# Kernel optimization log

Measured on AMD Instinct MI355X. Metric: run time of the kernel, lower is better.

## Reference

```python
import jax, jax.numpy as jnp
import numpy as np
from jax import lax

N = 100000      # nodes
E = 1600000     # edges
F_IN = 128      # nfeat
F_OUT = 32      # nhid


def _l2norm(v, eps=1e-12):
    return v / jnp.maximum(jnp.linalg.norm(v), eps)


def setup_inputs() -> dict:
    key = jax.random.key(0)
    k1, k2, k3, k4, k5 = jax.random.split(key, 5)
    x = jax.random.normal(k1, (N, F_IN), dtype=jnp.float32)
    edge_index = jax.random.randint(k2, (2, E), 0, N, dtype=jnp.int64)
    W = jax.random.normal(k3, (F_OUT, F_IN), dtype=jnp.float32) * (1.0 / np.sqrt(F_IN))
    bias = jax.random.normal(k4, (F_OUT,), dtype=jnp.float32) * 0.01
    prelu_a = jnp.full((1,), 0.25, dtype=jnp.float32)  # PReLU default init
    u_sn = jax.random.normal(k5, (F_OUT,), dtype=jnp.float32)
    return {"x": x, "edge_index": edge_index, "W": W, "bias": bias,
            "prelu_a": prelu_a, "u_sn": u_sn}


def _spectral_norm_weight(W, u):
    # one power iteration (torch default), u/v treated as buffers (no grad)
    v = lax.stop_gradient(_l2norm(W.T @ u))
    u2 = lax.stop_gradient(_l2norm(W @ v))
    sigma = jnp.dot(u2, W @ v)
    return W / sigma


def reference(x, edge_index, W, bias, prelu_a, u_sn):
    W_sn = _spectral_norm_weight(W, u_sn)
    # linear transform first (PyG GCNConv): [N, F_OUT]
    xw = x @ W_sn.T
    # add self loops
    loop = jnp.arange(N, dtype=edge_index.dtype)
    row = jnp.concatenate([edge_index[0], loop])  # source
    col = jnp.concatenate([edge_index[1], loop])  # target
    # symmetric normalization deg^{-1/2} A deg^{-1/2}, deg over targets
    deg = jax.ops.segment_sum(jnp.ones_like(col, dtype=xw.dtype), col, num_segments=N)
    dis = jnp.where(deg > 0, lax.rsqrt(deg), 0.0)
    norm = dis[row] * dis[col]                    # [E+N]
    # gather-scale-scatter aggregation
    msgs = xw[row] * norm[:, None]                # [E+N, F_OUT]
    out = jax.ops.segment_sum(msgs, col, num_segments=N)
    out = out + bias
    # PReLU with single shared slope
    a = prelu_a[0]
    return jnp.where(out >= 0, out, a * out)
```

## Files before the change

kernel.cpp:

```cpp
#include <hip/hip_runtime.h>
#include <hip/hip_fp16.h>

#define F_IN 128
#define F_OUT 32
#define PBLK 256
#define BSH 8

__global__ void k0_specnorm(const float* __restrict__ W, const float* __restrict__ u,
                            float* __restrict__ Wsc) {
    __shared__ float v[F_IN];
    __shared__ float red[F_IN];
    __shared__ float scal;
    int t = threadIdx.x;
    float acc = 0.f;
    for (int i = 0; i < F_OUT; ++i) acc += W[i * F_IN + t] * u[i];
    v[t] = acc;
    red[t] = acc * acc;
    __syncthreads();
    if (t == 0) {
        float s = 0.f;
        for (int i = 0; i < F_IN; ++i) s += red[i];
        scal = 1.0f / fmaxf(sqrtf(s), 1e-12f);
    }
    __syncthreads();
    v[t] = v[t] * scal;
    __syncthreads();
    if (t < F_OUT) {
        float a2 = 0.f;
        for (int j = 0; j < F_IN; ++j) a2 += W[t * F_IN + j] * v[j];
        red[t] = a2 * a2;
    }
    __syncthreads();
    if (t == 0) {
        float s = 0.f;
        for (int i = 0; i < F_OUT; ++i) s += red[i];
        scal = 1.0f / fmaxf(sqrtf(s), 1e-30f);
    }
    __syncthreads();
    float is = scal;
    for (int i = 0; i < F_OUT; ++i)
        Wsc[i * F_IN + t] = W[i * F_IN + t] * is;
}

__global__ __launch_bounds__(256) void k1_xw(const float* __restrict__ x,
                                             const float* __restrict__ Wsc,
                                             const float* __restrict__ dis,
                                             __half* __restrict__ xwh, int Nn) {
    __shared__ float xs[128 * 65];
    __shared__ float wt[128 * 32];
    int t = threadIdx.x;
    int rbase = blockIdx.x * 128;

    {
        int f = t >> 3;
        int kb = 16 * (t & 7);
        const float4* wrow = (const float4*)(Wsc + (size_t)f * F_IN + kb);
#pragma unroll
        for (int j = 0; j < 4; ++j) {
            float4 w = wrow[j];
            int k = kb + 4 * j;
            wt[(k + 0) * 32 + f] = w.x;
            wt[(k + 1) * 32 + f] = w.y;
            wt[(k + 2) * 32 + f] = w.z;
            wt[(k + 3) * 32 + f] = w.w;
        }
    }

    int r0 = (t >> 3) * 4;
    int f0 = (t & 7) * 4;
    float4 acc0 = {0, 0, 0, 0}, acc1 = {0, 0, 0, 0};
    float4 acc2 = {0, 0, 0, 0}, acc3 = {0, 0, 0, 0};
    const float4* wt4 = (const float4*)wt;
    int fq = f0 >> 2;

    for (int kc = 0; kc < 2; ++kc) {
        __syncthreads();
        {
            int rr = t >> 4;
            int k0 = 4 * (t & 15);
#pragma unroll
            for (int p = 0; p < 8; ++p) {
                int r = p * 16 + rr;
                int grow = rbase + r;
                if (grow >= Nn) grow = Nn - 1;
                float4 v = *(const float4*)(x + (size_t)grow * F_IN + kc * 64 + k0);
                xs[r * 65 + k0 + 0] = v.x;
                xs[r * 65 + k0 + 1] = v.y;
                xs[r * 65 + k0 + 2] = v.z;
                xs[r * 65 + k0 + 3] = v.w;
            }
        }
        __syncthreads();
#pragma unroll 4
        for (int kk = 0; kk < 64; ++kk) {
            int k = kc * 64 + kk;
            float4 w = wt4[k * 8 + fq];
            float x0 = xs[(r0 + 0) * 65 + kk];
            float x1 = xs[(r0 + 1) * 65 + kk];
            float x2 = xs[(r0 + 2) * 65 + kk];
            float x3 = xs[(r0 + 3) * 65 + kk];
            acc0.x += x0 * w.x; acc0.y += x0 * w.y; acc0.z += x0 * w.z; acc0.w += x0 * w.w;
            acc1.x += x1 * w.x; acc1.y += x1 * w.y; acc1.z += x1 * w.z; acc1.w += x1 * w.w;
            acc2.x += x2 * w.x; acc2.y += x2 * w.y; acc2.z += x2 * w.z; acc2.w += x2 * w.w;
            acc3.x += x3 * w.x; acc3.y += x3 * w.y; acc3.z += x3 * w.z; acc3.w += x3 * w.w;
        }
    }
    int g0 = rbase + r0;
#pragma unroll
    for (int q = 0; q < 4; ++q) {
        int g = g0 + q;
        if (g < Nn) {
            float d = dis[g];
            float4 a = (q == 0) ? acc0 : (q == 1) ? acc1 : (q == 2) ? acc2 : acc3;
            ushort4 s;
            s.x = __half_as_ushort(__float2half(a.x * d));
            s.y = __half_as_ushort(__float2half(a.y * d));
            s.z = __half_as_ushort(__float2half(a.z * d));
            s.w = __half_as_ushort(__float2half(a.w * d));
            *(ushort4*)(xwh + (size_t)g * F_OUT + f0) = s;
        }
    }
}

__global__ void k_hist(const int* __restrict__ col, int* __restrict__ M,
                       int E_, int NB) {
    __shared__ int h[512];
    int p = blockIdx.x, t = threadIdx.x;
    for (int b = t; b < NB; b += 256) h[b] = 0;
    __syncthreads();
    int epb = (E_ + PBLK - 1) / PBLK;
    int e0 = p * epb, e1 = min(e0 + epb, E_);
    for (int e = e0 + t; e < e1; e += 256)
        atomicAdd(&h[col[e] >> BSH], 1);
    __syncthreads();
    for (int b = t; b < NB; b += 256) M[b * PBLK + p] = h[b];
}

__global__ void k_scanA(int* __restrict__ M, int* __restrict__ total, int NB) {
    __shared__ int sd[256];
    int b = blockIdx.x, t = threadIdx.x;
    int v = M[b * PBLK + t];
    sd[t] = v;
    __syncthreads();
    for (int o = 1; o < 256; o <<= 1) {
        int u = (t >= o) ? sd[t - o] : 0;
        __syncthreads();
        sd[t] += u;
        __syncthreads();
    }
    M[b * PBLK + t] = sd[t] - v;
    if (t == 255) total[b] = sd[255];
}

__global__ void k_scanB(const int* __restrict__ total, int* __restrict__ base, int NB) {
    __shared__ int sd[512];
    int t = threadIdx.x;
    int v = (t < NB) ? total[t] : 0;
    sd[t] = v;
    __syncthreads();
    for (int o = 1; o < 512; o <<= 1) {
        int u = (t >= o) ? sd[t - o] : 0;
        __syncthreads();
        sd[t] += u;
        __syncthreads();
    }
    if (t < NB) base[t] = sd[t] - v;
    if (t == NB - 1) base[NB] = sd[t];
}

__global__ void k_scat1(const int* __restrict__ ei, const int* __restrict__ M,
                        const int* __restrict__ base, unsigned* __restrict__ staging,
                        int E_, int NB) {
    __shared__ int cur[512];
    int p = blockIdx.x, t = threadIdx.x;
    for (int b = t; b < NB; b += 256) cur[b] = base[b] + M[b * PBLK + p];
    __syncthreads();
    int epb = (E_ + PBLK - 1) / PBLK;
    int e0 = p * epb, e1 = min(e0 + epb, E_);
    for (int e = e0 + t; e < e1; e += 256) {
        int c = ei[E_ + e];
        int r = ei[e];
        int b = c >> BSH;
        int pos = atomicAdd(&cur[b], 1);
        staging[pos] = ((unsigned)r << BSH) | (unsigned)(c & 255);
    }
}

__global__ void k_sort2(const unsigned* __restrict__ staging, const int* __restrict__ base,
                        int* __restrict__ esr, float* __restrict__ dis,
                        int* __restrict__ cursor, int Nn, int E_, int NB) {
    __shared__ int hist[256];
    __shared__ int sd[256];
    __shared__ int lcur[256];
    int b = blockIdx.x, t = threadIdx.x;
    int nb0 = b << BSH;
    int nc = min(256, Nn - nb0);
    hist[t] = 0;
    __syncthreads();
    int s0 = base[b], s1 = base[b + 1];
    for (int j = s0 + t; j < s1; j += 256)
        atomicAdd(&hist[staging[j] & 255], 1);
    __syncthreads();
    int h = hist[t];
    if (t < nc) dis[nb0 + t] = rsqrtf((float)h + 1.0f);
    sd[t] = h;
    __syncthreads();
    for (int o = 1; o < 256; o <<= 1) {
        int u = (t >= o) ? sd[t - o] : 0;
        __syncthreads();
        sd[t] += u;
        __syncthreads();
    }
    int excl = sd[t] - h;
    if (t < nc) cursor[nb0 + t] = s0 + excl;
    if (b == NB - 1 && t == 0) cursor[Nn] = E_;
    lcur[t] = s0 + excl;
    __syncthreads();
    for (int j = s0 + t; j < s1; j += 256) {
        unsigned v = staging[j];
        int p = atomicAdd(&lcur[v & 255], 1);
        esr[p] = (int)(v >> BSH);
    }
}

__global__ void k4_gather(const int* __restrict__ esr, const int* __restrict__ cursor,
                          const __half* __restrict__ xws, const float* __restrict__ dis,
                          const float* __restrict__ bias, const float* __restrict__ pa,
                          float* __restrict__ out, int Nn) {
    int t = threadIdx.x;
    int node = blockIdx.x * 16 + (t >> 4);
    if (node >= Nn) return;
    int f2 = t & 15;
    int start = cursor[node], end = cursor[node + 1];
    float accx = 0.f, accy = 0.f;
    for (int j0 = start; j0 < end; j0 += 16) {
        int idx = j0 + f2;
        int rf = (idx < end) ? esr[idx] : 0;
        int m = end - j0;
        if (m > 16) m = 16;
        int i = 0;
        for (; i + 4 <= m; i += 4) {
            int r0 = __shfl(rf, i + 0, 16);
            int r1 = __shfl(rf, i + 1, 16);
            int r2 = __shfl(rf, i + 2, 16);
            int r3 = __shfl(rf, i + 3, 16);
            float2 a0 = __half22float2(*((const __half2*)(xws + (size_t)r0 * F_OUT) + f2));
            float2 a1 = __half22float2(*((const __half2*)(xws + (size_t)r1 * F_OUT) + f2));
            float2 a2 = __half22float2(*((const __half2*)(xws + (size_t)r2 * F_OUT) + f2));
            float2 a3 = __half22float2(*((const __half2*)(xws + (size_t)r3 * F_OUT) + f2));
            accx += a0.x + a1.x + a2.x + a3.x;
            accy += a0.y + a1.y + a2.y + a3.y;
        }
        for (; i < m; ++i) {
            int r = __shfl(rf, i, 16);
            float2 a = __half22float2(*((const __half2*)(xws + (size_t)r * F_OUT) + f2));
            accx += a.x;
            accy += a.y;
        }
    }
    float dc = dis[node];
    float2 self = __half22float2(*((const __half2*)(xws + (size_t)node * F_OUT) + f2));
    float2 bi = *((const float2*)bias + f2);
    float a = pa[0];
    float vx = (accx + self.x) * dc + bi.x;
    float vy = (accy + self.y) * dc + bi.y;
    float2 o;
    o.x = (vx >= 0.f) ? vx : a * vx;
    o.y = (vy >= 0.f) ? vy : a * vy;
    *((float2*)(out + (size_t)node * F_OUT) + f2) = o;
}

__global__ void k1_xw_f32(const float* __restrict__ x, const float* __restrict__ Wsc,
                          const float* __restrict__ dis, float* __restrict__ xw, int Nn) {
    int id = blockIdx.x * blockDim.x + threadIdx.x;
    if (id >= Nn * F_OUT) return;
    int r = id >> 5, f = id & 31;
    const float4* x4 = (const float4*)(x + (size_t)r * F_IN);
    const float4* w4 = (const float4*)(Wsc + (size_t)f * F_IN);
    float acc = 0.f;
#pragma unroll
    for (int k = 0; k < F_IN / 4; ++k) {
        float4 a = x4[k];
        float4 b = w4[k];
        acc += a.x * b.x + a.y * b.y + a.z * b.z + a.w * b.w;
    }
    xw[id] = acc * dis[r];
}

__global__ void k2_deg(const int* __restrict__ col, int* __restrict__ cnt, int E_) {
    int e = blockIdx.x * blockDim.x + threadIdx.x;
    if (e < E_) atomicAdd(&cnt[col[e]], 1);
}

__global__ void k3_dis(const int* __restrict__ cnt, float* __restrict__ dis, int Nn) {
    int i = blockIdx.x * blockDim.x + threadIdx.x;
    if (i < Nn) dis[i] = rsqrtf((float)cnt[i] + 1.0f);
}

__global__ void k4_scatter(const int* __restrict__ ei, const float* __restrict__ xws,
                           const float* __restrict__ dis, float* __restrict__ out, int E_) {
    int id = blockIdx.x * blockDim.x + threadIdx.x;
    if (id >= E_ * F_OUT) return;
    int e = id >> 5, f = id & 31;
    int r = ei[e];
    int c = ei[E_ + e];
    atomicAdd(&out[(size_t)c * F_OUT + f], xws[(size_t)r * F_OUT + f] * dis[c]);
}

__global__ void k5_epi(const float* __restrict__ xws, const float* __restrict__ dis,
                       const float* __restrict__ bias, const float* __restrict__ pa,
                       float* __restrict__ out, int Nn) {
    int id = blockIdx.x * blockDim.x + threadIdx.x;
    if (id >= Nn * F_OUT) return;
    int i = id >> 5, f = id & 31;
    float d = dis[i];
    float v = out[id] + xws[id] * d + bias[f];
    float a = pa[0];
    out[id] = (v >= 0.f) ? v : a * v;
}

extern "C" void kernel_launch(void* const* d_in, const int* in_sizes, int n_in,
                              void* d_out, int out_size, void* d_ws, size_t ws_size,
                              hipStream_t stream) {
    const float* x    = (const float*)d_in[0];
    const int*   ei   = (const int*)d_in[1];
    const float* W    = (const float*)d_in[2];
    const float* bias = (const float*)d_in[3];
    const float* pa   = (const float*)d_in[4];
    const float* u    = (const float*)d_in[5];

    int Nn = in_sizes[0] / F_IN;
    int E_ = in_sizes[1] / 2;
    float* out = (float*)d_out;

    int NB = (Nn + 255) >> BSH;

    size_t o = 0;
    __half*   xwh     = (__half*)d_ws;       o += (size_t)Nn * (F_OUT / 2);
    float*    Wsc     = (float*)d_ws + o;    o += F_OUT * F_IN;
    float*    dis     = (float*)d_ws + o;    o += Nn;
    int*      cursor  = (int*)d_ws + o;      o += Nn + 1;
    int*      M       = (int*)d_ws + o;      o += (size_t)NB * PBLK;
    int*      total   = (int*)d_ws + o;      o += NB;
    int*      base    = (int*)d_ws + o;      o += NB + 1;
    unsigned* staging = (unsigned*)d_ws + o; o += E_;
    int*      esr     = (int*)d_ws + o;      o += E_;
    bool big_ws = (ws_size >= o * sizeof(float)) && (NB <= 512);

    if (big_ws) {
        k0_specnorm<<<1, 128, 0, stream>>>(W, u, Wsc);
        k_hist<<<PBLK, 256, 0, stream>>>(ei + E_, M, E_, NB);
        k_scanA<<<NB, 256, 0, stream>>>(M, total, NB);
        k_scanB<<<1, 512, 0, stream>>>(total, base, NB);
        k_scat1<<<PBLK, 256, 0, stream>>>(ei, M, base, staging, E_, NB);
        k_sort2<<<NB, 256, 0, stream>>>(staging, base, esr, dis, cursor, Nn, E_, NB);
        k1_xw<<<(Nn + 127) / 128, 256, 0, stream>>>(x, Wsc, dis, xwh, Nn);
        k4_gather<<<(Nn + 15) / 16, 256, 0, stream>>>(esr, cursor, xwh, dis, bias, pa, out, Nn);
    } else {
        size_t o2 = 0;
        float* xw2  = (float*)d_ws;       o2 += (size_t)Nn * F_OUT;
        float* Wsc2 = (float*)d_ws + o2;  o2 += F_OUT * F_IN;
        float* dis2 = (float*)d_ws + o2;  o2 += Nn;
        int*   deg2 = (int*)d_ws + o2;    o2 += Nn;
        hipMemsetAsync(deg2, 0, (size_t)Nn * sizeof(int), stream);
        hipMemsetAsync(d_out, 0, (size_t)Nn * F_OUT * sizeof(float), stream);
        k0_specnorm<<<1, 128, 0, stream>>>(W, u, Wsc2);
        k2_deg<<<(E_ + 255) / 256, 256, 0, stream>>>(ei + E_, deg2, E_);
        k3_dis<<<(Nn + 255) / 256, 256, 0, stream>>>(deg2, dis2, Nn);
        int nT1 = Nn * F_OUT;
        k1_xw_f32<<<(nT1 + 255) / 256, 256, 0, stream>>>(x, Wsc2, dis2, xw2, Nn);
        int nT4 = E_ * F_OUT;
        k4_scatter<<<(nT4 + 255) / 256, 256, 0, stream>>>(ei, xw2, dis2, out, E_);
        k5_epi<<<(nT1 + 255) / 256, 256, 0, stream>>>(xw2, dis2, bias, pa, out, Nn);
    }
}
```

Before: 182.4 us.

## Fuse CSR build into one cooperative kernel and aggregate via shared-memory atomics

Merges spectral norm, the per-block histogram, both scans, the bucket scatter and the degree count into a single cooperative kernel that uses grid syncs, so there are fewer launches. The bucket size drops from 256 to 128 nodes. The second sort pass that built per-node CSR is removed, and aggregation now accumulates each bucket's messages directly into a 128x32 shared-memory tile with float atomics. This cuts launch overhead and the esr/cursor pass, but adds shared-atomic contention and grid-sync costs, and 256 blocks of cooperative work may serialize the histogram.

```diff
diff --git a/kernel.cpp b/kernel.cpp
--- a/kernel.cpp
+++ b/kernel.cpp
@@ -1,45 +1,134 @@
 #include <hip/hip_runtime.h>
 #include <hip/hip_fp16.h>
+#include <hip/hip_cooperative_groups.h>
+namespace cg = cooperative_groups;
 
 #define F_IN 128
 #define F_OUT 32
-#define PBLK 256
-#define BSH 8
-
-__global__ void k0_specnorm(const float* __restrict__ W, const float* __restrict__ u,
-                            float* __restrict__ Wsc) {
-    __shared__ float v[F_IN];
-    __shared__ float red[F_IN];
-    __shared__ float scal;
-    int t = threadIdx.x;
-    float acc = 0.f;
-    for (int i = 0; i < F_OUT; ++i) acc += W[i * F_IN + t] * u[i];
-    v[t] = acc;
-    red[t] = acc * acc;
-    __syncthreads();
-    if (t == 0) {
-        float s = 0.f;
-        for (int i = 0; i < F_IN; ++i) s += red[i];
-        scal = 1.0f / fmaxf(sqrtf(s), 1e-12f);
-    }
-    __syncthreads();
-    v[t] = v[t] * scal;
-    __syncthreads();
-    if (t < F_OUT) {
-        float a2 = 0.f;
-        for (int j = 0; j < F_IN; ++j) a2 += W[t * F_IN + j] * v[j];
-        red[t] = a2 * a2;
-    }
-    __syncthreads();
-    if (t == 0) {
-        float s = 0.f;
-        for (int i = 0; i < F_OUT; ++i) s += red[i];
-        scal = 1.0f / fmaxf(sqrtf(s), 1e-30f);
-    }
-    __syncthreads();
-    float is = scal;
-    for (int i = 0; i < F_OUT; ++i)
-        Wsc[i * F_IN + t] = W[i * F_IN + t] * is;
+#define BSH 7
+#define BMSK 127
+#define MAXNB 2048
+
+__global__ __launch_bounds__(256) void k_coop(
+    const float* __restrict__ W, const float* __restrict__ u, float* __restrict__ Wsc,
+    const int* __restrict__ ei, int* __restrict__ M, int* __restrict__ Mex,
+    int* __restrict__ total, int* __restrict__ base,
+    unsigned* __restrict__ staging, float* __restrict__ dis,
+    int E_, int Nn, int NB) {
+    cg::grid_group grid = cg::this_grid();
+    __shared__ int smi[MAXNB];
+    __shared__ int sd[256];
+    __shared__ float sv[F_IN];
+    __shared__ float sr[F_IN];
+    __shared__ float ssc;
+    int p = blockIdx.x, t = threadIdx.x;
+    int epb = (E_ + 254) / 255;
+
+    if (p == 0) {
+        if (t < F_IN) {
+            float acc = 0.f;
+            for (int i = 0; i < F_OUT; ++i) acc += W[i * F_IN + t] * u[i];
+            sv[t] = acc; sr[t] = acc * acc;
+        }
+        __syncthreads();
+        if (t == 0) {
+            float s = 0.f;
+            for (int i = 0; i < F_IN; ++i) s += sr[i];
+            ssc = 1.0f / fmaxf(sqrtf(s), 1e-12f);
+        }
+        __syncthreads();
+        if (t < F_IN) sv[t] *= ssc;
+        __syncthreads();
+        if (t < F_OUT) {
+            float a2 = 0.f;
+            for (int j = 0; j < F_IN; ++j) a2 += W[t * F_IN + j] * sv[j];
+            sr[t] = a2 * a2;
+        }
+        __syncthreads();
+        if (t == 0) {
+            float s = 0.f;
+            for (int i = 0; i < F_OUT; ++i) s += sr[i];
+            ssc = 1.0f / fmaxf(sqrtf(s), 1e-30f);
+        }
+        __syncthreads();
+        if (t < F_IN) {
+            float is = ssc;
+            for (int i = 0; i < F_OUT; ++i) Wsc[i * F_IN + t] = W[i * F_IN + t] * is;
+        }
+        for (int b = t; b < NB; b += 256) M[b] = 0;
+    } else {
+        for (int b = t; b < NB; b += 256) smi[b] = 0;
+        __syncthreads();
+        int e0 = (p - 1) * epb, e1 = min(e0 + epb, E_);
+        const int* col = ei + E_;
+        for (int e = e0 + t; e < e1; e += 256)
+            atomicAdd(&smi[col[e] >> BSH], 1);
+        __syncthreads();
+        int* Mp = M + (size_t)p * MAXNB;
+        for (int b = t; b < NB; b += 256) Mp[b] = smi[b];
+    }
+    grid.sync();
+
+    for (int b = p; b < NB; b += 256) {
+        int v = M[(size_t)t * MAXNB + b];
+        sd[t] = v;
+        __syncthreads();
+        for (int o = 1; o < 256; o <<= 1) {
+            int uu = (t >= o) ? sd[t - o] : 0;
+            __syncthreads();
+            sd[t] += uu;
+            __syncthreads();
+        }
+        Mex[(size_t)b * 256 + t] = sd[t] - v;
+        if (t == 255) total[b] = sd[255];
+        __syncthreads();
+    }
+    grid.sync();
+
+    if (p == 0) {
+        int C = (NB + 255) / 256;
+        int i0 = t * C, i1 = min(i0 + C, NB);
+        int s = 0;
+        for (int i = i0; i < i1; ++i) s += total[i];
+        int tsum = s;
+        sd[t] = s;
+        __syncthreads();
+        for (int o = 1; o < 256; o <<= 1) {
+            int uu = (t >= o) ? sd[t - o] : 0;
+            __syncthreads();
+            sd[t] += uu;
+            __syncthreads();
+        }
+        int run = sd[t] - tsum;
+        for (int i = i0; i < i1; ++i) { base[i] = run; run += total[i]; }
+        if (t == 255) base[NB] = sd[255];
+    }
+    grid.sync();
+
+    if (p > 0) {
+        for (int b = t; b < NB; b += 256) smi[b] = base[b] + Mex[(size_t)b * 256 + p];
+        __syncthreads();
+        int e0 = (p - 1) * epb, e1 = min(e0 + epb, E_);
+        for (int e = e0 + t; e < e1; e += 256) {
+            int c = ei[E_ + e];
+            int r = ei[e];
+            int pos = atomicAdd(&smi[c >> BSH], 1);
+            staging[pos] = ((unsigned)r << BSH) | (unsigned)(c & BMSK);
+        }
+    }
+    grid.sync();
+
+    for (int b = p; b < NB; b += 256) {
+        if (t < 128) smi[t] = 0;
+        __syncthreads();
+        int s0 = base[b], s1 = base[b + 1];
+        for (int jj = s0 + t; jj < s1; jj += 256)
+            atomicAdd(&smi[staging[jj] & BMSK], 1);
+        __syncthreads();
+        int nb0 = b << BSH;
+        if (t < 128 && nb0 + t < Nn) dis[nb0 + t] = rsqrtf((float)smi[t] + 1.0f);
+        __syncthreads();
+    }
 }
 
 __global__ __launch_bounds__(256) void k1_xw(const float* __restrict__ x,
@@ -79,8 +168,8 @@
             int rr = t >> 4;
             int k0 = 4 * (t & 15);
 #pragma unroll
-            for (int p = 0; p < 8; ++p) {
-                int r = p * 16 + rr;
+            for (int pi = 0; pi < 8; ++pi) {
+                int r = pi * 16 + rr;
                 int grow = rbase + r;
                 if (grow >= Nn) grow = Nn - 1;
                 float4 v = *(const float4*)(x + (size_t)grow * F_IN + kc * 64 + k0);
@@ -122,152 +211,83 @@
     }
 }
 
-__global__ void k_hist(const int* __restrict__ col, int* __restrict__ M,
-                       int E_, int NB) {
-    __shared__ int h[512];
-    int p = blockIdx.x, t = threadIdx.x;
-    for (int b = t; b < NB; b += 256) h[b] = 0;
-    __syncthreads();
-    int epb = (E_ + PBLK - 1) / PBLK;
-    int e0 = p * epb, e1 = min(e0 + epb, E_);
-    for (int e = e0 + t; e < e1; e += 256)
-        atomicAdd(&h[col[e] >> BSH], 1);
-    __syncthreads();
-    for (int b = t; b < NB; b += 256) M[b * PBLK + p] = h[b];
-}
-
-__global__ void k_scanA(int* __restrict__ M, int* __restrict__ total, int NB) {
-    __shared__ int sd[256];
-    int b = blockIdx.x, t = threadIdx.x;
-    int v = M[b * PBLK + t];
-    sd[t] = v;
-    __syncthreads();
-    for (int o = 1; o < 256; o <<= 1) {
-        int u = (t >= o) ? sd[t - o] : 0;
-        __syncthreads();
-        sd[t] += u;
-        __syncthreads();
-    }
-    M[b * PBLK + t] = sd[t] - v;
-    if (t == 255) total[b] = sd[255];
-}
-
-__global__ void k_scanB(const int* __restrict__ total, int* __restrict__ base, int NB) {
-    __shared__ int sd[512];
-    int t = threadIdx.x;
-    int v = (t < NB) ? total[t] : 0;
-    sd[t] = v;
-    __syncthreads();
-    for (int o = 1; o < 512; o <<= 1) {
-        int u = (t >= o) ? sd[t - o] : 0;
-        __syncthreads();
-        sd[t] += u;
-        __syncthreads();
-    }
-    if (t < NB) base[t] = sd[t] - v;
-    if (t == NB - 1) base[NB] = sd[t];
-}
-
-__global__ void k_scat1(const int* __restrict__ ei, const int* __restrict__ M,
-                        const int* __restrict__ base, unsigned* __restrict__ staging,
-                        int E_, int NB) {
-    __shared__ int cur[512];
-    int p = blockIdx.x, t = threadIdx.x;
-    for (int b = t; b < NB; b += 256) cur[b] = base[b] + M[b * PBLK + p];
-    __syncthreads();
-    int epb = (E_ + PBLK - 1) / PBLK;
-    int e0 = p * epb, e1 = min(e0 + epb, E_);
-    for (int e = e0 + t; e < e1; e += 256) {
-        int c = ei[E_ + e];
-        int r = ei[e];
-        int b = c >> BSH;
-        int pos = atomicAdd(&cur[b], 1);
-        staging[pos] = ((unsigned)r << BSH) | (unsigned)(c & 255);
-    }
-}
-
-__global__ void k_sort2(const unsigned* __restrict__ staging, const int* __restrict__ base,
-                        int* __restrict__ esr, float* __restrict__ dis,
-                        int* __restrict__ cursor, int Nn, int E_, int NB) {
-    __shared__ int hist[256];
-    __shared__ int sd[256];
-    __shared__ int lcur[256];
+__global__ __launch_bounds__(256) void k_gather(const unsigned* __restrict__ staging,
+        const int* __restrict__ base, const __half* __restrict__ xwh,
+        const float* __restrict__ dis, const float* __restrict__ bias,
+        const float* __restrict__ pa, float* __restrict__ out, int Nn) {
+    __shared__ float acc[128 * 32];
     int b = blockIdx.x, t = threadIdx.x;
     int nb0 = b << BSH;
-    int nc = min(256, Nn - nb0);
-    hist[t] = 0;
+    int nc = min(128, Nn - nb0);
+    for (int i = t; i < 128 * 32; i += 256) acc[i] = 0.f;
     __syncthreads();
     int s0 = base[b], s1 = base[b + 1];
-    for (int j = s0 + t; j < s1; j += 256)
-        atomicAdd(&hist[staging[j] & 255], 1);
-    __syncthreads();
-    int h = hist[t];
-    if (t < nc) dis[nb0 + t] = rsqrtf((float)h + 1.0f);
-    sd[t] = h;
-    __syncthreads();
-    for (int o = 1; o < 256; o <<= 1) {
-        int u = (t >= o) ? sd[t - o] : 0;
-        __syncthreads();
-        sd[t] += u;
-        __syncthreads();
-    }
-    int excl = sd[t] - h;
-    if (t < nc) cursor[nb0 + t] = s0 + excl;
-    if (b == NB - 1 && t == 0) cursor[Nn] = E_;
-    lcur[t] = s0 + excl;
-    __syncthreads();
-    for (int j = s0 + t; j < s1; j += 256) {
-        unsigned v = staging[j];
-        int p = atomicAdd(&lcur[v & 255], 1);
-        esr[p] = (int)(v >> BSH);
-    }
-}
-
-__global__ void k4_gather(const int* __restrict__ esr, const int* __restrict__ cursor,
-                          const __half* __restrict__ xws, const float* __restrict__ dis,
-                          const float* __restrict__ bias, const float* __restrict__ pa,
-                          float* __restrict__ out, int Nn) {
+    int g = t >> 4, f2 = t & 15;
+    int j = s0 + g;
+    for (; j + 16 < s1; j += 32) {
+        unsigned v0 = staging[j];
+        unsigned v1 = staging[j + 16];
+        int c0 = v0 & BMSK, r0 = (int)(v0 >> BSH);
+        int c1 = v1 & BMSK, r1 = (int)(v1 >> BSH);
+        float2 a0 = __half22float2(*((const __half2*)(xwh + (size_t)r0 * F_OUT) + f2));
+        float2 a1 = __half22float2(*((const __half2*)(xwh + (size_t)r1 * F_OUT) + f2));
+        atomicAdd(&acc[c0 * 32 + 2 * f2],     a0.x);
+        atomicAdd(&acc[c0 * 32 + 2 * f2 + 1], a0.y);
+        atomicAdd(&acc[c1 * 32 + 2 * f2],     a1.x);
+        atomicAdd(&acc[c1 * 32 + 2 * f2 + 1], a1.y);
+    }
+    if (j < s1) {
+        unsigned v0 = staging[j];
+        int c0 = v0 & BMSK, r0 = (int)(v0 >> BSH);
+        float2 a0 = __half22float2(*((const __half2*)(xwh + (size_t)r0 * F_OUT) + f2));
+        atomicAdd(&acc[c0 * 32 + 2 * f2],     a0.x);
+        atomicAdd(&acc[c0 * 32 + 2 * f2 + 1], a0.y);
+    }
+    __syncthreads();
+    float aslope = pa[0];
+    for (int idx = t; idx < nc * 32; idx += 256) {
+        int node = nb0 + (idx >> 5);
+        int f = idx & 31;
+        float dc = dis[node];
+        float s = __half2float(xwh[(size_t)node * F_OUT + f]);
+        float v = (acc[idx] + s) * dc + bias[f];
+        out[(size_t)node * F_OUT + f] = (v >= 0.f) ? v : aslope * v;
+    }
+}
+
+__global__ void k0_specnorm(const float* __restrict__ W, const float* __restrict__ u,
+                            float* __restrict__ Wsc) {
+    __shared__ float v[F_IN];
+    __shared__ float red[F_IN];
+    __shared__ float scal;
     int t = threadIdx.x;
-    int node = blockIdx.x * 16 + (t >> 4);
-    if (node >= Nn) return;
-    int f2 = t & 15;
-    int start = cursor[node], end = cursor[node + 1];
-    float accx = 0.f, accy = 0.f;
-    for (int j0 = start; j0 < end; j0 += 16) {
-        int idx = j0 + f2;
-        int rf = (idx < end) ? esr[idx] : 0;
-        int m = end - j0;
-        if (m > 16) m = 16;
-        int i = 0;
-        for (; i + 4 <= m; i += 4) {
-            int r0 = __shfl(rf, i + 0, 16);
-            int r1 = __shfl(rf, i + 1, 16);
-            int r2 = __shfl(rf, i + 2, 16);
-            int r3 = __shfl(rf, i + 3, 16);
-            float2 a0 = __half22float2(*((const __half2*)(xws + (size_t)r0 * F_OUT) + f2));
-            float2 a1 = __half22float2(*((const __half2*)(xws + (size_t)r1 * F_OUT) + f2));
-            float2 a2 = __half22float2(*((const __half2*)(xws + (size_t)r2 * F_OUT) + f2));
-            float2 a3 = __half22float2(*((const __half2*)(xws + (size_t)r3 * F_OUT) + f2));
-            accx += a0.x + a1.x + a2.x + a3.x;
-            accy += a0.y + a1.y + a2.y + a3.y;
-        }
-        for (; i < m; ++i) {
-            int r = __shfl(rf, i, 16);
-            float2 a = __half22float2(*((const __half2*)(xws + (size_t)r * F_OUT) + f2));
-            accx += a.x;
-            accy += a.y;
-        }
-    }
-    float dc = dis[node];
-    float2 self = __half22float2(*((const __half2*)(xws + (size_t)node * F_OUT) + f2));
-    float2 bi = *((const float2*)bias + f2);
-    float a = pa[0];
-    float vx = (accx + self.x) * dc + bi.x;
-    float vy = (accy + self.y) * dc + bi.y;
-    float2 o;
-    o.x = (vx >= 0.f) ? vx : a * vx;
-    o.y = (vy >= 0.f) ? vy : a * vy;
-    *((float2*)(out + (size_t)node * F_OUT) + f2) = o;
+    float acc = 0.f;
+    for (int i = 0; i < F_OUT; ++i) acc += W[i * F_IN + t] * u[i];
+    v[t] = acc; red[t] = acc * acc;
+    __syncthreads();
+    if (t == 0) {
+        float s = 0.f;
+        for (int i = 0; i < F_IN; ++i) s += red[i];
+        scal = 1.0f / fmaxf(sqrtf(s), 1e-12f);
+    }
+    __syncthreads();
+    v[t] *= scal;
+    __syncthreads();
+    if (t < F_OUT) {
+        float a2 = 0.f;
+        for (int j = 0; j < F_IN; ++j) a2 += W[t * F_IN + j] * v[j];
+        red[t] = a2 * a2;
+    }
+    __syncthreads();
+    if (t == 0) {
+        float s = 0.f;
+        for (int i = 0; i < F_OUT; ++i) s += red[i];
+        scal = 1.0f / fmaxf(sqrtf(s), 1e-30f);
+    }
+    __syncthreads();
+    float is = scal;
+    for (int i = 0; i < F_OUT; ++i)
+        Wsc[i * F_IN + t] = W[i * F_IN + t] * is;
 }
 
 __global__ void k1_xw_f32(const float* __restrict__ x, const float* __restrict__ Wsc,
@@ -333,29 +353,28 @@
     int E_ = in_sizes[1] / 2;
     float* out = (float*)d_out;
 
-    int NB = (Nn + 255) >> BSH;
+    int NB = (Nn + BMSK) >> BSH;
 
     size_t o = 0;
     __half*   xwh     = (__half*)d_ws;       o += (size_t)Nn * (F_OUT / 2);
     float*    Wsc     = (float*)d_ws + o;    o += F_OUT * F_IN;
     float*    dis     = (float*)d_ws + o;    o += Nn;
-    int*      cursor  = (int*)d_ws + o;      o += Nn + 1;
-    int*      M       = (int*)d_ws + o;      o += (size_t)NB * PBLK;
+    int*      M       = (int*)d_ws + o;      o += (size_t)256 * MAXNB;
+    int*      Mex     = (int*)d_ws + o;      o += (size_t)NB * 256;
     int*      total   = (int*)d_ws + o;      o += NB;
     int*      base    = (int*)d_ws + o;      o += NB + 1;
     unsigned* staging = (unsigned*)d_ws + o; o += E_;
-    int*      esr     = (int*)d_ws + o;      o += E_;
-    bool big_ws = (ws_size >= o * sizeof(float)) && (NB <= 512);
+    bool big_ws = (ws_size >= o * sizeof(float)) && (NB <= MAXNB);
 
     if (big_ws) {
-        k0_specnorm<<<1, 128, 0, stream>>>(W, u, Wsc);
-        k_hist<<<PBLK, 256, 0, stream>>>(ei + E_, M, E_, NB);
-        k_scanA<<<NB, 256, 0, stream>>>(M, total, NB);
-        k_scanB<<<1, 512, 0, stream>>>(total, base, NB);
-        k_scat1<<<PBLK, 256, 0, stream>>>(ei, M, base, staging, E_, NB);
-        k_sort2<<<NB, 256, 0, stream>>>(staging, base, esr, dis, cursor, Nn, E_, NB);
+        void* args[] = {(void*)&W, (void*)&u, (void*)&Wsc, (void*)&ei,
+                        (void*)&M, (void*)&Mex, (void*)&total, (void*)&base,
+                        (void*)&staging, (void*)&dis,
+                        (void*)&E_, (void*)&Nn, (void*)&NB};
+        hipLaunchCooperativeKernel((const void*)k_coop, dim3(256), dim3(256),
+                                   args, 0, stream);
         k1_xw<<<(Nn + 127) / 128, 256, 0, stream>>>(x, Wsc, dis, xwh, Nn);
-        k4_gather<<<(Nn + 15) / 16, 256, 0, stream>>>(esr, cursor, xwh, dis, bias, pa, out, Nn);
+        k_gather<<<NB, 256, 0, stream>>>(staging, base, xwh, dis, bias, pa, out, Nn);
     } else {
         size_t o2 = 0;
         float* xw2  = (float*)d_ws;       o2 += (size_t)Nn * F_OUT;
```

Measured after the change: 625.2 us. 243% more time.

## Fuse spectral norm, histogram and XW into one kernel; merge scans into scatter

Applied to the files above, without the earlier changes.

Each XW block now recomputes the spectral-norm scale redundantly and also builds its slice of the column-bucket histogram. This drops the separate specnorm and hist launches and the serial dependency between them. The second-level scan over bucket totals is folded into the scatter kernel, and the histogram partition count now matches the XW grid. Because XW no longer waits for the degree computation, the dis scaling of source rows moves into the gather, which costs one extra dis load per edge. Every block also repeats the small power-iteration work.

```diff
diff --git a/kernel.cpp b/kernel.cpp
--- a/kernel.cpp
+++ b/kernel.cpp
@@ -3,66 +3,74 @@
 
 #define F_IN 128
 #define F_OUT 32
-#define PBLK 256
 #define BSH 8
-
-__global__ void k0_specnorm(const float* __restrict__ W, const float* __restrict__ u,
-                            float* __restrict__ Wsc) {
-    __shared__ float v[F_IN];
-    __shared__ float red[F_IN];
-    __shared__ float scal;
-    int t = threadIdx.x;
-    float acc = 0.f;
-    for (int i = 0; i < F_OUT; ++i) acc += W[i * F_IN + t] * u[i];
-    v[t] = acc;
-    red[t] = acc * acc;
-    __syncthreads();
-    if (t == 0) {
-        float s = 0.f;
-        for (int i = 0; i < F_IN; ++i) s += red[i];
-        scal = 1.0f / fmaxf(sqrtf(s), 1e-12f);
-    }
-    __syncthreads();
-    v[t] = v[t] * scal;
-    __syncthreads();
-    if (t < F_OUT) {
-        float a2 = 0.f;
-        for (int j = 0; j < F_IN; ++j) a2 += W[t * F_IN + j] * v[j];
-        red[t] = a2 * a2;
-    }
-    __syncthreads();
-    if (t == 0) {
-        float s = 0.f;
-        for (int i = 0; i < F_OUT; ++i) s += red[i];
-        scal = 1.0f / fmaxf(sqrtf(s), 1e-30f);
-    }
-    __syncthreads();
-    float is = scal;
-    for (int i = 0; i < F_OUT; ++i)
-        Wsc[i * F_IN + t] = W[i * F_IN + t] * is;
-}
-
-__global__ __launch_bounds__(256) void k1_xw(const float* __restrict__ x,
-                                             const float* __restrict__ Wsc,
-                                             const float* __restrict__ dis,
-                                             __half* __restrict__ xwh, int Nn) {
+#define BMSK 255
+
+__global__ __launch_bounds__(256) void k1h(
+    const float* __restrict__ x, const float* __restrict__ W,
+    const float* __restrict__ u, const int* __restrict__ ei,
+    __half* __restrict__ xwh, int* __restrict__ M,
+    int Nn, int E_, int NB, int P) {
     __shared__ float xs[128 * 65];
     __shared__ float wt[128 * 32];
+    __shared__ int   smi[512];
+    __shared__ float sv[F_IN];
+    __shared__ float sr[F_IN];
+    __shared__ float ssc;
     int t = threadIdx.x;
-    int rbase = blockIdx.x * 128;
-
+    int p = blockIdx.x;
+
+    for (int b = t; b < NB; b += 256) smi[b] = 0;
+    __syncthreads();
+    int epb = (E_ + P - 1) / P;
+    int e0 = p * epb, e1 = min(e0 + epb, E_);
+    const int* col = ei + E_;
+    for (int e = e0 + t; e < e1; e += 256)
+        atomicAdd(&smi[col[e] >> BSH], 1);
+    __syncthreads();
+    for (int b = t; b < NB; b += 256) M[(size_t)p * NB + b] = smi[b];
+
+    if (t < F_IN) {
+        float a = 0.f;
+        for (int i = 0; i < F_OUT; ++i) a += W[i * F_IN + t] * u[i];
+        sv[t] = a; sr[t] = a * a;
+    }
+    __syncthreads();
+    for (int o = 64; o > 0; o >>= 1) {
+        if (t < o) sr[t] += sr[t + o];
+        __syncthreads();
+    }
+    if (t == 0) ssc = 1.0f / fmaxf(sqrtf(sr[0]), 1e-12f);
+    __syncthreads();
+    if (t < F_IN) sv[t] *= ssc;
+    __syncthreads();
+    if (t < F_OUT) {
+        float a = 0.f;
+        for (int j = 0; j < F_IN; ++j) a += W[t * F_IN + j] * sv[j];
+        sr[t] = a * a;
+    }
+    __syncthreads();
+    for (int o = 16; o > 0; o >>= 1) {
+        if (t < o) sr[t] += sr[t + o];
+        __syncthreads();
+    }
+    if (t == 0) ssc = 1.0f / fmaxf(sqrtf(sr[0]), 1e-30f);
+    __syncthreads();
+    float is = ssc;
+
+    int rbase = p * 128;
     {
         int f = t >> 3;
         int kb = 16 * (t & 7);
-        const float4* wrow = (const float4*)(Wsc + (size_t)f * F_IN + kb);
+        const float4* wrow = (const float4*)(W + (size_t)f * F_IN + kb);
 #pragma unroll
         for (int j = 0; j < 4; ++j) {
             float4 w = wrow[j];
             int k = kb + 4 * j;
-            wt[(k + 0) * 32 + f] = w.x;
-            wt[(k + 1) * 32 + f] = w.y;
-            wt[(k + 2) * 32 + f] = w.z;
-            wt[(k + 3) * 32 + f] = w.w;
+            wt[(k + 0) * 32 + f] = w.x * is;
+            wt[(k + 1) * 32 + f] = w.y * is;
+            wt[(k + 2) * 32 + f] = w.z * is;
+            wt[(k + 3) * 32 + f] = w.w * is;
         }
     }
 
@@ -79,8 +87,8 @@
             int rr = t >> 4;
             int k0 = 4 * (t & 15);
 #pragma unroll
-            for (int p = 0; p < 8; ++p) {
-                int r = p * 16 + rr;
+            for (int pi = 0; pi < 8; ++pi) {
+                int r = pi * 16 + rr;
                 int grow = rbase + r;
                 if (grow >= Nn) grow = Nn - 1;
                 float4 v = *(const float4*)(x + (size_t)grow * F_IN + kc * 64 + k0);
@@ -110,37 +118,34 @@
     for (int q = 0; q < 4; ++q) {
         int g = g0 + q;
         if (g < Nn) {
-            float d = dis[g];
             float4 a = (q == 0) ? acc0 : (q == 1) ? acc1 : (q == 2) ? acc2 : acc3;
             ushort4 s;
-            s.x = __half_as_ushort(__float2half(a.x * d));
-            s.y = __half_as_ushort(__float2half(a.y * d));
-            s.z = __half_as_ushort(__float2half(a.z * d));
-            s.w = __half_as_ushort(__float2half(a.w * d));
+            s.x = __half_as_ushort(__float2half(a.x));
+            s.y = __half_as_ushort(__float2half(a.y));
+            s.z = __half_as_ushort(__float2half(a.z));
+            s.w = __half_as_ushort(__float2half(a.w));
             *(ushort4*)(xwh + (size_t)g * F_OUT + f0) = s;
         }
     }
 }
 
-__global__ void k_hist(const int* __restrict__ col, int* __restrict__ M,
-                       int E_, int NB) {
-    __shared__ int h[512];
-    int p = blockIdx.x, t = threadIdx.x;
-    for (int b = t; b < NB; b += 256) h[b] = 0;
-    __syncthreads();
-    int epb = (E_ + PBLK - 1) / PBLK;
-    int e0 = p * epb, e1 = min(e0 + epb, E_);
-    for (int e = e0 + t; e < e1; e += 256)
-        atomicAdd(&h[col[e] >> BSH], 1);
-    __syncthreads();
-    for (int b = t; b < NB; b += 256) M[b * PBLK + p] = h[b];
-}
-
-__global__ void k_scanA(int* __restrict__ M, int* __restrict__ total, int NB) {
+__global__ __launch_bounds__(256) void k_scanA(int* __restrict__ M,
+                                               int* __restrict__ total,
+                                               int NB, int P) {
     __shared__ int sd[256];
     int b = blockIdx.x, t = threadIdx.x;
-    int v = M[b * PBLK + t];
-    sd[t] = v;
+    int C = (P + 255) >> 8;
+    int vals[8];
+    int run = 0;
+#pragma unroll 4
+    for (int j = 0; j < C; ++j) {
+        int p = t * C + j;
+        int v = (p < P) ? M[(size_t)p * NB + b] : 0;
+        vals[j] = run;
+        run += v;
+    }
+    int tsum = run;
+    sd[t] = tsum;
     __syncthreads();
     for (int o = 1; o < 256; o <<= 1) {
         int u = (t >= o) ? sd[t - o] : 0;
@@ -148,47 +153,68 @@
         sd[t] += u;
         __syncthreads();
     }
-    M[b * PBLK + t] = sd[t] - v;
+    int cb = sd[t] - tsum;
+#pragma unroll 4
+    for (int j = 0; j < C; ++j) {
+        int p = t * C + j;
+        if (p < P) M[(size_t)p * NB + b] = cb + vals[j];
+    }
     if (t == 255) total[b] = sd[255];
 }
 
-__global__ void k_scanB(const int* __restrict__ total, int* __restrict__ base, int NB) {
-    __shared__ int sd[512];
-    int t = threadIdx.x;
-    int v = (t < NB) ? total[t] : 0;
-    sd[t] = v;
-    __syncthreads();
-    for (int o = 1; o < 512; o <<= 1) {
+__global__ __launch_bounds__(256) void k_scat1(
+    const int* __restrict__ ei, const int* __restrict__ M,
+    const int* __restrict__ total, int* __restrict__ base,
+    unsigned* __restrict__ staging, int E_, int NB, int P) {
+    __shared__ int scur[512];
+    __shared__ int sd[256];
+    int p = blockIdx.x, t = threadIdx.x;
+    int C = (NB + 255) >> 8;
+    int vals[2];
+    int run = 0;
+#pragma unroll
+    for (int j = 0; j < 2; ++j) {
+        int b = t * C + j;
+        int v = (j < C && b < NB) ? total[b] : 0;
+        vals[j] = run;
+        run += v;
+    }
+    int tsum = run;
+    sd[t] = tsum;
+    __syncthreads();
+    for (int o = 1; o < 256; o <<= 1) {
         int u = (t >= o) ? sd[t - o] : 0;
         __syncthreads();
         sd[t] += u;
         __syncthreads();
     }
-    if (t < NB) base[t] = sd[t] - v;
-    if (t == NB - 1) base[NB] = sd[t];
-}
-
-__global__ void k_scat1(const int* __restrict__ ei, const int* __restrict__ M,
-                        const int* __restrict__ base, unsigned* __restrict__ staging,
-                        int E_, int NB) {
-    __shared__ int cur[512];
-    int p = blockIdx.x, t = threadIdx.x;
-    for (int b = t; b < NB; b += 256) cur[b] = base[b] + M[b * PBLK + p];
-    __syncthreads();
-    int epb = (E_ + PBLK - 1) / PBLK;
+    int cb = sd[t] - tsum;
+#pragma unroll
+    for (int j = 0; j < 2; ++j) {
+        int b = t * C + j;
+        if (j < C && b < NB) {
+            int sb = cb + vals[j];
+            scur[b] = sb + M[(size_t)p * NB + b];
+            if (p == 0) base[b] = sb;
+        }
+    }
+    if (p == 0 && t == 255) base[NB] = sd[255];
+    __syncthreads();
+    int epb = (E_ + P - 1) / P;
     int e0 = p * epb, e1 = min(e0 + epb, E_);
+    const int* col = ei + E_;
     for (int e = e0 + t; e < e1; e += 256) {
-        int c = ei[E_ + e];
+        int c = col[e];
         int r = ei[e];
-        int b = c >> BSH;
-        int pos = atomicAdd(&cur[b], 1);
-        staging[pos] = ((unsigned)r << BSH) | (unsigned)(c & 255);
-    }
-}
-
-__global__ void k_sort2(const unsigned* __restrict__ staging, const int* __restrict__ base,
-                        int* __restrict__ esr, float* __restrict__ dis,
-                        int* __restrict__ cursor, int Nn, int E_, int NB) {
+        int pos = atomicAdd(&scur[c >> BSH], 1);
+        staging[pos] = ((unsigned)r << BSH) | (unsigned)(c & BMSK);
+    }
+}
+
+__global__ __launch_bounds__(256) void k_sort2(
+    const unsigned* __restrict__ staging, const int* __restrict__ base,
+    int* __restrict__ esr, float* __restrict__ dis,
+    int* __restrict__ cursor, int Nn, int E_, int NB) {
     __shared__ int hist[256];
     __shared__ int sd[256];
     __shared__ int lcur[256];
@@ -199,7 +225,7 @@
     __syncthreads();
     int s0 = base[b], s1 = base[b + 1];
     for (int j = s0 + t; j < s1; j += 256)
-        atomicAdd(&hist[staging[j] & 255], 1);
+        atomicAdd(&hist[staging[j] & BMSK], 1);
     __syncthreads();
     int h = hist[t];
     if (t < nc) dis[nb0 + t] = rsqrtf((float)h + 1.0f);
@@ -218,15 +244,16 @@
     __syncthreads();
     for (int j = s0 + t; j < s1; j += 256) {
         unsigned v = staging[j];
-        int p = atomicAdd(&lcur[v & 255], 1);
-        esr[p] = (int)(v >> BSH);
-    }
-}
-
-__global__ void k4_gather(const int* __restrict__ esr, const int* __restrict__ cursor,
-                          const __half* __restrict__ xws, const float* __restrict__ dis,
-                          const float* __restrict__ bias, const float* __restrict__ pa,
-                          float* __restrict__ out, int Nn) {
+        int pp = atomicAdd(&lcur[v & BMSK], 1);
+        esr[pp] = (int)(v >> BSH);
+    }
+}
+
+__global__ __launch_bounds__(256) void k_gather(
+    const int* __restrict__ esr, const int* __restrict__ cursor,
+    const __half* __restrict__ xwh, const float* __restrict__ dis,
+    const float* __restrict__ bias, const float* __restrict__ pa,
+    float* __restrict__ out, int Nn) {
     int t = threadIdx.x;
     int node = blockIdx.x * 16 + (t >> 4);
     if (node >= Nn) return;
@@ -244,30 +271,67 @@
             int r1 = __shfl(rf, i + 1, 16);
             int r2 = __shfl(rf, i + 2, 16);
             int r3 = __shfl(rf, i + 3, 16);
-            float2 a0 = __half22float2(*((const __half2*)(xws + (size_t)r0 * F_OUT) + f2));
-            float2 a1 = __half22float2(*((const __half2*)(xws + (size_t)r1 * F_OUT) + f2));
-            float2 a2 = __half22float2(*((const __half2*)(xws + (size_t)r2 * F_OUT) + f2));
-            float2 a3 = __half22float2(*((const __half2*)(xws + (size_t)r3 * F_OUT) + f2));
-            accx += a0.x + a1.x + a2.x + a3.x;
-            accy += a0.y + a1.y + a2.y + a3.y;
+            float d0 = dis[r0], d1 = dis[r1], d2 = dis[r2], d3 = dis[r3];
+            float2 a0 = __half22float2(*((const __half2*)(xwh + (size_t)r0 * F_OUT) + f2));
+            float2 a1 = __half22float2(*((const __half2*)(xwh + (size_t)r1 * F_OUT) + f2));
+            float2 a2 = __half22float2(*((const __half2*)(xwh + (size_t)r2 * F_OUT) + f2));
+            float2 a3 = __half22float2(*((const __half2*)(xwh + (size_t)r3 * F_OUT) + f2));
+            accx += a0.x * d0 + a1.x * d1 + a2.x * d2 + a3.x * d3;
+            accy += a0.y * d0 + a1.y * d1 + a2.y * d2 + a3.y * d3;
         }
         for (; i < m; ++i) {
             int r = __shfl(rf, i, 16);
-            float2 a = __half22float2(*((const __half2*)(xws + (size_t)r * F_OUT) + f2));
-            accx += a.x;
-            accy += a.y;
+            float d = dis[r];
+            float2 a = __half22float2(*((const __half2*)(xwh + (size_t)r * F_OUT) + f2));
+            accx += a.x * d;
+            accy += a.y * d;
         }
     }
     float dc = dis[node];
-    float2 self = __half22float2(*((const __half2*)(xws + (size_t)node * F_OUT) + f2));
+    float2 self = __half22float2(*((const __half2*)(xwh + (size_t)node * F_OUT) + f2));
     float2 bi = *((const float2*)bias + f2);
     float a = pa[0];
-    float vx = (accx + self.x) * dc + bi.x;
-    float vy = (accy + self.y) * dc + bi.y;
+    float vx = (accx + self.x * dc) * dc + bi.x;
+    float vy = (accy + self.y * dc) * dc + bi.y;
     float2 o;
     o.x = (vx >= 0.f) ? vx : a * vx;
     o.y = (vy >= 0.f) ? vy : a * vy;
     *((float2*)(out + (size_t)node * F_OUT) + f2) = o;
+}
+
+__global__ void k0_specnorm(const float* __restrict__ W, const float* __restrict__ u,
+                            float* __restrict__ Wsc) {
+    __shared__ float v[F_IN];
+    __shared__ float red[F_IN];
+    __shared__ float scal;
+    int t = threadIdx.x;
+    float acc = 0.f;
+    for (int i = 0; i < F_OUT; ++i) acc += W[i * F_IN + t] * u[i];
+    v[t] = acc; red[t] = acc * acc;
+    __syncthreads();
+    if (t == 0) {
+        float s = 0.f;
+        for (int i = 0; i < F_IN; ++i) s += red[i];
+        scal = 1.0f / fmaxf(sqrtf(s), 1e-12f);
+    }
+    __syncthreads();
+    v[t] *= scal;
+    __syncthreads();
+    if (t < F_OUT) {
+        float a2 = 0.f;
+        for (int j = 0; j < F_IN; ++j) a2 += W[t * F_IN + j] * v[j];
+        red[t] = a2 * a2;
+    }
+    __syncthreads();
+    if (t == 0) {
+        float s = 0.f;
+        for (int i = 0; i < F_OUT; ++i) s += red[i];
+        scal = 1.0f / fmaxf(sqrtf(s), 1e-30f);
+    }
+    __syncthreads();
+    float is = scal;
+    for (int i = 0; i < F_OUT; ++i)
+        Wsc[i * F_IN + t] = W[i * F_IN + t] * is;
 }
 
 __global__ void k1_xw_f32(const float* __restrict__ x, const float* __restrict__ Wsc,
@@ -333,29 +397,26 @@
     int E_ = in_sizes[1] / 2;
     float* out = (float*)d_out;
 
-    int NB = (Nn + 255) >> BSH;
+    int NB = (Nn + BMSK) >> BSH;
+    int P  = (Nn + 127) / 128;
 
     size_t o = 0;
     __half*   xwh     = (__half*)d_ws;       o += (size_t)Nn * (F_OUT / 2);
-    float*    Wsc     = (float*)d_ws + o;    o += F_OUT * F_IN;
     float*    dis     = (float*)d_ws + o;    o += Nn;
     int*      cursor  = (int*)d_ws + o;      o += Nn + 1;
-    int*      M       = (int*)d_ws + o;      o += (size_t)NB * PBLK;
+    int*      M       = (int*)d_ws + o;      o += (size_t)P * NB;
     int*      total   = (int*)d_ws + o;      o += NB;
     int*      base    = (int*)d_ws + o;      o += NB + 1;
     unsigned* staging = (unsigned*)d_ws + o; o += E_;
     int*      esr     = (int*)d_ws + o;      o += E_;
-    bool big_ws = (ws_size >= o * sizeof(float)) && (NB <= 512);
+    bool big_ws = (ws_size >= o * sizeof(float)) && (NB <= 512) && (P <= 2048);
 
     if (big_ws) {
-        k0_specnorm<<<1, 128, 0, stream>>>(W, u, Wsc);
-        k_hist<<<PBLK, 256, 0, stream>>>(ei + E_, M, E_, NB);
-        k_scanA<<<NB, 256, 0, stream>>>(M, total, NB);
-        k_scanB<<<1, 512, 0, stream>>>(total, base, NB);
-        k_scat1<<<PBLK, 256, 0, stream>>>(ei, M, base, staging, E_, NB);
+        k1h<<<P, 256, 0, stream>>>(x, W, u, ei, xwh, M, Nn, E_, NB, P);
+        k_scanA<<<NB, 256, 0, stream>>>(M, total, NB, P);
+        k_scat1<<<P, 256, 0, stream>>>(ei, M, total, base, staging, E_, NB, P);
         k_sort2<<<NB, 256, 0, stream>>>(staging, base, esr, dis, cursor, Nn, E_, NB);
-        k1_xw<<<(Nn + 127) / 128, 256, 0, stream>>>(x, Wsc, dis, xwh, Nn);
-        k4_gather<<<(Nn + 15) / 16, 256, 0, stream>>>(esr, cursor, xwh, dis, bias, pa, out, Nn);
+        k_gather<<<(Nn + 15) / 16, 256, 0, stream>>>(esr, cursor, xwh, dis, bias, pa, out, Nn);
     } else {
         size_t o2 = 0;
         float* xw2  = (float*)d_ws;       o2 += (size_t)Nn * F_OUT;
```

Result: slower. 189.3 us (+3.8%).
